# Performance work log

Hardware: AMD Instinct MI355X
Metric: run time of the kernel (lower is better)

The kernel has to match this reference:

```python
import jax, jax.numpy as jnp
import numpy as np

B, T, L = 64, 60, 49
EMBED, HID, VOCAB = 768, 768, 10000


def setup_inputs() -> dict:
    key = jax.random.key(0)
    ks = jax.random.split(key, 17)
    def n(k, shape, s=1.0):
        return jax.random.normal(k, shape, dtype=jnp.float32) * s
    W = 0.02  # param init scale
    return {
        "x": n(ks[0], (B, T, 2 * EMBED)),
        "hiddens": n(ks[1], (B, T, HID)),
        "cells": n(ks[2], (B, T, HID)),
        "G": n(ks[3], (B, L, HID)),
        "H": n(ks[4], (B, L, HID)),
        # Sentinel params (bias=False)
        "W_sx": n(ks[5], (HID, 2 * EMBED), W),
        "W_sh": n(ks[6], (HID, HID), W),
        # SwitchableAttention params
        "W_ax": n(ks[7], (HID, 2 * EMBED), W),
        "W_ah": n(ks[8], (HID, HID), W),
        "W_ag": n(ks[9], (HID, HID), W),
        "w_switch": n(ks[10], (1, HID), W),
        # Atten (adaptive attention) params, bias=False
        "Wv": n(ks[11], (L, HID), W),
        "Wg": n(ks[12], (L, HID), W),
        "Ws": n(ks[13], (L, HID), W),
        "wh": n(ks[14], (1, L), W),
        # output MLP
        "W_mlp": n(ks[15], (VOCAB, HID), W),
        "b_mlp": jnp.zeros((VOCAB,), dtype=jnp.float32),
    }


def reference(x, hiddens, cells, G, H, W_sx, W_sh, W_ax, W_ah, W_ag,
              w_switch, Wv, Wg, Ws, wh, W_mlp, b_mlp):
    # Dropout layers are treated as identity (eval mode).
    b, t, _ = x.shape
    # h_{t-1}: zero initial hidden prepended, last step dropped
    h0 = jnp.zeros((b, 1, HID), dtype=hiddens.dtype)
    hiddens_t_1 = jnp.concatenate([h0, hiddens[:, :-1, :]], axis=1)

    # Sentinel gate: sigmoid(Wx x + Wh h_{t-1}) * tanh(c_t)
    gate = jax.nn.sigmoid(jnp.einsum('bte,he->bth', x, W_sx)
                          + jnp.einsum('btk,hk->bth', hiddens_t_1, W_sh))
    s_t = gate * jnp.tanh(cells)  # [B,T,HID]

    # SwitchableAttention: gate between visual H and guidance G per region,
    # conditioned on pooled word context x.
    q = jnp.einsum('bte,he->bth', x, W_ax).mean(axis=1)  # [B,HID]
    sH = jnp.einsum('blh,oh->blo', jnp.tanh(jnp.einsum('blh,kh->blk', H, W_ah) + q[:, None, :]), w_switch)  # [B,L,1]
    sG = jnp.einsum('blh,oh->blo', jnp.tanh(jnp.einsum('blh,kh->blk', G, W_ag) + q[:, None, :]), w_switch)  # [B,L,1]
    switch_weights = jax.nn.softmax(jnp.concatenate([sH, sG], axis=-1), axis=-1)  # [B,L,2]
    V = switch_weights[..., 0:1] * H + switch_weights[..., 1:2] * G  # [B,L,HID]

    # Adaptive attention (Atten): spatial attention + visual sentinel
    pv = jnp.einsum('blh,kh->blk', V, Wv)        # [B,L,49]
    pg = jnp.einsum('bth,kh->btk', hiddens, Wg)  # [B,T,49]
    z_t = jnp.einsum('btlk,ok->btlo', jnp.tanh(pv[:, None, :, :] + pg[:, :, None, :]), wh)[..., 0]  # [B,T,L]
    alpha = jax.nn.softmax(z_t, axis=-1)  # [B,T,L]
    z_s = jnp.einsum('btk,ok->bto', jnp.tanh(jnp.einsum('bth,kh->btk', s_t, Ws) + pg), wh)  # [B,T,1]
    alpha_hat = jax.nn.softmax(jnp.concatenate([z_t, z_s], axis=-1), axis=-1)  # [B,T,L+1]
    beta = alpha_hat[..., -1:]  # [B,T,1]
    c_t = jnp.einsum('btl,blh->bth', alpha, V)
    c_hat = beta * s_t + (1.0 - beta) * c_t

    scores = jnp.einsum('bth,vh->btv', c_hat + hiddens, W_mlp) + b_mlp  # [B,T,VOCAB]
    return scores, alpha, beta, switch_weights
```

## Files before the change

### kernel.cpp

```cpp
#include <hip/hip_runtime.h>

#define BB 64
#define TT 60
#define LL 49
#define HID 768
#define E2 1536
#define VOC 10000
#define BT (BB*TT)
#define BL (BB*LL)
#define NPAD_MLP 10240
#define NPAD_S 128

typedef __bf16 bf16x8 __attribute__((ext_vector_type(8)));
typedef float f32x4 __attribute__((ext_vector_type(4)));

__device__ __forceinline__ unsigned short f2bf(float f) {
  union { float f; unsigned int u; } v; v.f = f;
  unsigned int u = v.u;
  return (unsigned short)((u + 0x7fffu + ((u >> 16) & 1u)) >> 16);
}
__device__ __forceinline__ float bf2f(unsigned short h) {
  union { unsigned int u; float f; } v; v.u = ((unsigned int)h) << 16;
  return v.f;
}
__device__ __forceinline__ float fast_tanh(float x) {
  float e = __expf(2.f * x);
  return 1.f - 2.f / (e + 1.f);
}
__device__ __forceinline__ float fast_sigmoid(float x) {
  return 1.f / (1.f + __expf(-x));
}

#define NSEG 14
#define CHUNK4 2048
struct SegT {
  const float* src;
  unsigned short* dst;
  int n4;
  int nrows;
  int mode;
  int blk0;
};
struct SegTable { SegT s[NSEG]; };

__global__ __launch_bounds__(256) void k_convall(SegTable tab) {
  int b = blockIdx.x;
  int si = 0;
#pragma unroll
  for (int i = 1; i < NSEG; ++i) si += (b >= tab.s[i].blk0);
  SegT sg = tab.s[si];
  int lb = b - sg.blk0;
  int end = (lb + 1) * CHUNK4; end = end < sg.n4 ? end : sg.n4;
  for (int i = lb * CHUNK4 + threadIdx.x; i < end; i += 256) {
    ushort4 o; o.x = o.y = o.z = o.w = 0;
    if (sg.mode == 0) {
      float4 v = ((const float4*)sg.src)[i];
      o.x = f2bf(v.x); o.y = f2bf(v.y); o.z = f2bf(v.z); o.w = f2bf(v.w);
    } else if (sg.mode == 1) {
      int row = i / 192;
      if (row < sg.nrows) {
        float4 v = ((const float4*)sg.src)[i];
        o.x = f2bf(v.x); o.y = f2bf(v.y); o.z = f2bf(v.z); o.w = f2bf(v.w);
      }
    } else {
      int bt = i / 192;
      if (bt % TT != 0) {
        float4 v = ((const float4*)sg.src)[i - 192];
        o.x = f2bf(v.x); o.y = f2bf(v.y); o.z = f2bf(v.z); o.w = f2bf(v.w);
      }
    }
    ((ushort4*)sg.dst)[i] = o;
  }
}

__global__ __launch_bounds__(256) void k_xmean(const float* __restrict__ x,
                                               unsigned short* __restrict__ xm) {
  int b = blockIdx.x / 6;
  int c = (blockIdx.x % 6) * 256 + threadIdx.x;
  float s = 0.f;
  for (int t = 0; t < TT; ++t) s += x[((size_t)b * TT + t) * E2 + c];
  xm[(size_t)b * E2 + c] = f2bf(s * (1.f / 60.f));
}

struct SSeg {
  const unsigned short* A; const unsigned short* B; float* C;
  int M, Nout, K, nMblk, blk0;
};
#define NSSEG 3
struct SSegTable { SSeg s[NSSEG]; };

__global__ __launch_bounds__(256) void gemm_bt_seg(SSegTable tab)
{
  __shared__ __attribute__((aligned(16))) unsigned short As[128*32];
  __shared__ __attribute__((aligned(16))) unsigned short Bs[128*32];
  const int tid  = threadIdx.x;
  const int lane = tid & 63;
  const int wave = tid >> 6;

  const int nwg = gridDim.x;
  const int id  = blockIdx.x;
  const int q = nwg >> 3, r = nwg & 7;
  const int xcd = id & 7, lo = id >> 3;
  const int wgid = (xcd < r ? xcd * (q + 1) : r * (q + 1) + (xcd - r) * q) + lo;

  int si = 0;
#pragma unroll
  for (int i = 1; i < NSSEG; ++i) si += (wgid >= tab.s[i].blk0);
  const SSeg sg = tab.s[si];
  const int lwg = wgid - sg.blk0;
  const int mb = lwg % sg.nMblk;
  const int nb = lwg / sg.nMblk;
  const int M = sg.M, Nout = sg.Nout, K = sg.K;
  const unsigned short* __restrict__ A  = sg.A;
  const unsigned short* __restrict__ Bw = sg.B;
  float* __restrict__ C = sg.C;
  const int m0 = mb * 128;
  const int n0 = nb * 128;
  const int wm = (wave >> 1) * 64;
  const int wn = (wave & 1) * 64;

  f32x4 acc[4][4];
#pragma unroll
  for (int i = 0; i < 4; ++i)
#pragma unroll
    for (int j = 0; j < 4; ++j) acc[i][j] = f32x4{0.f, 0.f, 0.f, 0.f};

  const int lrow = lane & 15;
  const int kb   = (lane >> 4) * 8;

  for (int k0 = 0; k0 < K; k0 += 32) {
    __syncthreads();
#pragma unroll
    for (int p = 0; p < 2; ++p) {
      int slot = p * 256 + wave * 64 + lane;
      int row = slot >> 2, c8 = slot & 3;
      int ar = m0 + row; ar = ar < M ? ar : (M - 1);
      const unsigned short* asrc = A + (size_t)ar * K + k0 + c8 * 8;
      __builtin_amdgcn_global_load_lds(
          (const __attribute__((address_space(1))) void*)asrc,
          (__attribute__((address_space(3))) void*)&As[(p * 256 + wave * 64) * 8],
          16, 0, 0);
      const unsigned short* bsrc = Bw + (size_t)(n0 + row) * K + k0 + c8 * 8;
      __builtin_amdgcn_global_load_lds(
          (const __attribute__((address_space(1))) void*)bsrc,
          (__attribute__((address_space(3))) void*)&Bs[(p * 256 + wave * 64) * 8],
          16, 0, 0);
    }
    __syncthreads();

    bf16x8 av[4], bv[4];
#pragma unroll
    for (int i = 0; i < 4; ++i)
      av[i] = *(const bf16x8*)&As[(wm + i * 16 + lrow) * 32 + kb];
#pragma unroll
    for (int j = 0; j < 4; ++j)
      bv[j] = *(const bf16x8*)&Bs[(wn + j * 16 + lrow) * 32 + kb];
#pragma unroll
    for (int i = 0; i < 4; ++i)
#pragma unroll
      for (int j = 0; j < 4; ++j)
        acc[i][j] = __builtin_amdgcn_mfma_f32_16x16x32_bf16(av[i], bv[j], acc[i][j], 0, 0, 0);
  }

  const int cr = (lane >> 4) * 4;
  const int cc = lane & 15;
#pragma unroll
  for (int i = 0; i < 4; ++i) {
    int row0 = m0 + wm + i * 16 + cr;
#pragma unroll
    for (int j = 0; j < 4; ++j) {
      int col = n0 + wn + j * 16 + cc;
      if (col < Nout) {
#pragma unroll
        for (int r2 = 0; r2 < 4; ++r2) {
          int row = row0 + r2;
          if (row < M) C[(size_t)row * Nout + col] = acc[i][j][r2];
        }
      }
    }
  }
}

#define BARR() do { asm volatile("" ::: "memory"); __builtin_amdgcn_s_barrier(); \
                    asm volatile("" ::: "memory"); } while (0)
#define VM4() asm volatile("s_waitcnt vmcnt(4)" ::: "memory")
#define VM0() asm volatile("s_waitcnt vmcnt(0)" ::: "memory")

#define STAGE1(bufi, op, kt) do {                                               \
  int k0_ = (kt) * 32;                                                          \
  _Pragma("unroll")                                                             \
  for (int l_ = 0; l_ < 2; ++l_) {                                              \
    int rr_ = l_ * 128 + sr0;                                                   \
    int ss_ = ssp ^ ((rr_ >> 1) & 3);                                           \
    int gr_;                                                                    \
    if (op) gr_ = n0 + rr_;                                                     \
    else    gr_ = CLAMP ? ((m0 + rr_) < M ? (m0 + rr_) : (M - 1)) : (m0 + rr_); \
    const unsigned short* src_ = ((op) ? Bw : Ap) + (size_t)gr_ * K + k0_ + ss_ * 8; \
    char* dst_ = smem + (bufi) * 32768 + (op) * 16384 + l_ * 8192 + w * 1024;   \
    __builtin_amdgcn_global_load_lds(                                           \
        (const __attribute__((address_space(1))) void*)src_,                    \
        (__attribute__((address_space(3))) void*)dst_, 16, 0, 0);               \
  }                                                                             \
} while (0)

#define LDA(bufi, row) (*(const bf16x8*)(smem + (bufi) * 32768 + (row) * 64 + (cg ^ (((row) >> 1) & 3)) * 16))
#define LDB(bufi, row) (*(const bf16x8*)(smem + (bufi) * 32768 + 16384 + (row) * 64 + (cg ^ (((row) >> 1) & 3)) * 16))

#define PH0(bufi, STAGE_STMT) do {                                              \
  STAGE_STMT;                                                                   \
  bfr0 = LDB(bufi, wn + lrow);                                                  \
  bfr1 = LDB(bufi, wn + 16 + lrow);                                             \
  _Pragma("unroll")                                                             \
  for (int i_ = 0; i_ < 8; ++i_) afr[i_] = LDA(bufi, wm + i_ * 16 + lrow);      \
  __builtin_amdgcn_s_setprio(1);                                                \
  _Pragma("unroll")                                                             \
  for (int i_ = 0; i_ < 8; ++i_) {                                              \
    acc[i_][0] = __builtin_amdgcn_mfma_f32_16x16x32_bf16(afr[i_], bfr0, acc[i_][0], 0, 0, 0); \
    acc[i_][1] = __builtin_amdgcn_mfma_f32_16x16x32_bf16(afr[i_], bfr1, acc[i_][1], 0, 0, 0); \
  }                                                                             \
  __builtin_amdgcn_s_setprio(0);                                                \
  BARR();                                                                       \
} while (0)

#define PH1(bufi, STAGE_STMT, VM_STMT) do {                                     \
  STAGE_STMT;                                                                   \
  bfr0 = LDB(bufi, wn + 32 + lrow);                                             \
  bfr1 = LDB(bufi, wn + 48 + lrow);                                             \
  __builtin_amdgcn_s_setprio(1);                                                \
  _Pragma("unroll")                                                             \
  for (int i_ = 0; i_ < 8; ++i_) {                                              \
    acc[i_][2] = __builtin_amdgcn_mfma_f32_16x16x32_bf16(afr[i_], bfr0, acc[i_][2], 0, 0, 0); \
    acc[i_][3] = __builtin_amdgcn_mfma_f32_16x16x32_bf16(afr[i_], bfr1, acc[i_][3], 0, 0, 0); \
  }                                                                             \
  __builtin_amdgcn_s_setprio(0);                                                \
  VM_STMT;                                                                      \
  BARR();                                                                       \
} while (0)

struct GSeg {
  const unsigned short* A; const unsigned short* B; float* C;
  const float* bias;
  int M, Nout, K, nMblk, blk0;
};
#define NGSEG 5
struct GSegTable { GSeg s[NGSEG]; };

template <bool CLAMP>
__global__ __launch_bounds__(512, 2) void gemm8p(GSegTable tab)
{
  extern __shared__ char smem[];
  const int tid  = threadIdx.x;
  const int lane = tid & 63;
  const int w    = tid >> 6;
  const int lrow = lane & 15;
  const int cg   = lane >> 4;
  const int sr0  = w * 16 + (lane >> 2);
  const int ssp  = lane & 3;

  const int nwg = gridDim.x;
  const int id  = blockIdx.x;
  const int q = nwg >> 3, r = nwg & 7;
  const int xcd = id & 7, lo = id >> 3;
  const int wgid = (xcd < r ? xcd * (q + 1) : r * (q + 1) + (xcd - r) * q) + lo;

  int si = 0;
#pragma unroll
  for (int i = 1; i < NGSEG; ++i) si += (wgid >= tab.s[i].blk0);
  const GSeg sg = tab.s[si];
  const int lwg = wgid - sg.blk0;
  const int mb = lwg % sg.nMblk;
  const int nb = lwg / sg.nMblk;
  const int M = sg.M, Nout = sg.Nout, K = sg.K;
  const unsigned short* __restrict__ Ap = sg.A;
  const unsigned short* __restrict__ Bw = sg.B;
  float* __restrict__ C = sg.C;
  const float* __restrict__ bias = sg.bias;

  const int m0 = mb * 256;
  const int n0 = nb * 256;
  const int wm = (w >> 2) * 128;
  const int wn = (w & 3) * 64;

  f32x4 acc[8][4];
#pragma unroll
  for (int i = 0; i < 8; ++i)
#pragma unroll
    for (int j = 0; j < 4; ++j) acc[i][j] = f32x4{0.f, 0.f, 0.f, 0.f};
  bf16x8 afr[8];
  bf16x8 bfr0, bfr1;

  const int NT = K >> 5;

  STAGE1(0, 0, 0);
  STAGE1(0, 1, 0);
  STAGE1(1, 0, 1);
  STAGE1(1, 1, 1);
  VM4();
  BARR();

  int b = 0;
  for (int kt = 0; kt < NT - 2; ++kt) {
    int b2 = b + 2; if (b2 >= 3) b2 -= 3;
    PH0(b, STAGE1(b2, 0, kt + 2));
    PH1(b, STAGE1(b2, 1, kt + 2), VM4(););
    ++b; if (b == 3) b = 0;
  }
  PH0(b, ;);
  PH1(b, ;, VM0(););
  ++b; if (b == 3) b = 0;
  PH0(b, ;);
  {
    bfr0 = LDB(b, wn + 32 + lrow);
    bfr1 = LDB(b, wn + 48 + lrow);
#pragma unroll
    for (int i_ = 0; i_ < 8; ++i_) {
      acc[i_][2] = __builtin_amdgcn_mfma_f32_16x16x32_bf16(afr[i_], bfr0, acc[i_][2], 0, 0, 0);
      acc[i_][3] = __builtin_amdgcn_mfma_f32_16x16x32_bf16(afr[i_], bfr1, acc[i_][3], 0, 0, 0);
    }
  }

#pragma unroll
  for (int i = 0; i < 8; ++i) {
    int row0 = m0 + wm + i * 16 + (lane >> 4) * 4;
#pragma unroll
    for (int j = 0; j < 4; ++j) {
      int col = n0 + wn + j * 16 + (lane & 15);
      if (col < Nout) {
        float badd = bias ? bias[col] : 0.f;
#pragma unroll
        for (int r2 = 0; r2 < 4; ++r2) {
          int row = row0 + r2;
          if (!CLAMP || row < M) C[(size_t)row * Nout + col] = acc[i][j][r2] + badd;
        }
      }
    }
  }
}

__global__ void k_st(const float* __restrict__ XS, const float* __restrict__ HS,
                     const float* __restrict__ cells, unsigned short* __restrict__ stbf, int n) {
  int i = blockIdx.x * blockDim.x + threadIdx.x;
  int stride = gridDim.x * blockDim.x;
  for (; i < n; i += stride) {
    float pre = XS[i] + HS[i];
    float v = fast_sigmoid(pre) * fast_tanh(cells[i]);
    stbf[i] = f2bf(v);
  }
}

__global__ __launch_bounds__(256) void k_switch(
    const float* __restrict__ AH, const float* __restrict__ AG,
    const float* __restrict__ q, const float* __restrict__ wsw,
    const float* __restrict__ H, const float* __restrict__ G,
    unsigned short* __restrict__ Vbf, float* __restrict__ sw_out)
{
  int bl = blockIdx.x;
  int b = bl / LL;
  int tid = threadIdx.x;
  float aH = 0.f, aG = 0.f;
  for (int h = tid; h < HID; h += 256) {
    float qv = q[b * HID + h], w = wsw[h];
    aH += fast_tanh(AH[(size_t)bl * HID + h] + qv) * w;
    aG += fast_tanh(AG[(size_t)bl * HID + h] + qv) * w;
  }
#pragma unroll
  for (int off = 32; off > 0; off >>= 1) {
    aH += __shfl_down(aH, off);
    aG += __shfl_down(aG, off);
  }
  __shared__ float redH[4], redG[4];
  int lane = tid & 63, wave = tid >> 6;
  if (lane == 0) { redH[wave] = aH; redG[wave] = aG; }
  __syncthreads();
  float sH = redH[0] + redH[1] + redH[2] + redH[3];
  float sG = redG[0] + redG[1] + redG[2] + redG[3];
  float m = fmaxf(sH, sG);
  float e0 = __expf(sH - m), e1 = __expf(sG - m);
  float inv = 1.f / (e0 + e1);
  float sw0 = e0 * inv, sw1 = e1 * inv;
  if (tid == 0) { sw_out[bl * 2] = sw0; sw_out[bl * 2 + 1] = sw1; }
  for (int h = tid; h < HID; h += 256) {
    float v = sw0 * H[(size_t)bl * HID + h] + sw1 * G[(size_t)bl * HID + h];
    Vbf[(size_t)bl * HID + h] = f2bf(v);
  }
}

__global__ __launch_bounds__(256) void k_attn(
    const float* __restrict__ PV, const float* __restrict__ PG,
    const float* __restrict__ SS, const float* __restrict__ wh,
    const unsigned short* __restrict__ stbf, const unsigned short* __restrict__ Vbf,
    const float* __restrict__ hiddens,
    float* __restrict__ alpha_out, float* __restrict__ beta_out,
    unsigned short* __restrict__ chh)
{
  const int TG = 4;
  int b  = blockIdx.x / (TT / TG);
  int t0 = (blockIdx.x % (TT / TG)) * TG;
  int tid = threadIdx.x;
  __shared__ float pg_s[TG][LL], wh_s[LL], zz[TG][LL + 1], alpha_s[TG][LL], beta_sh[TG];

  if (tid < LL) wh_s[tid] = wh[tid];
  if (tid < TG * LL) {
    int tt = tid / LL, k = tid - tt * LL;
    pg_s[tt][k] = PG[(size_t)(b * TT + t0 + tt) * 64 + k];
  }
  __syncthreads();

  if (tid < TG * (LL + 1)) {
    int tt = tid / (LL + 1), l = tid - tt * (LL + 1);
    const float* src = (l < LL) ? &PV[((size_t)b * LL + l) * 64]
                                : &SS[(size_t)(b * TT + t0 + tt) * 64];
    float acc = 0.f;
    for (int k = 0; k < LL; ++k) acc += fast_tanh(src[k] + pg_s[tt][k]) * wh_s[k];
    zz[tt][l] = acc;
  }
  __syncthreads();

  if (tid < TG) {
    int tt = tid, bt = b * TT + t0 + tt;
    float mx = -1e30f;
    for (int l = 0; l < LL; ++l) mx = fmaxf(mx, zz[tt][l]);
    float sum = 0.f;
    for (int l = 0; l < LL; ++l) { float e = __expf(zz[tt][l] - mx); alpha_s[tt][l] = e; sum += e; }
    float inv = 1.f / sum;
    for (int l = 0; l < LL; ++l) {
      alpha_s[tt][l] *= inv;
      alpha_out[(size_t)bt * LL + l] = alpha_s[tt][l];
    }
    float mx2 = fmaxf(mx, zz[tt][LL]);
    float s2 = 0.f;
    for (int l = 0; l <= LL; ++l) s2 += __expf(zz[tt][l] - mx2);
    float bet = __expf(zz[tt][LL] - mx2) / s2;
    beta_sh[tt] = bet;
    beta_out[bt] = bet;
  }
  __syncthreads();

  for (int h = tid; h < HID; h += 256) {
    float ct[TG] = {0.f, 0.f, 0.f, 0.f};
    for (int l = 0; l < LL; ++l) {
      float v = bf2f(Vbf[((size_t)b * LL + l) * HID + h]);
#pragma unroll
      for (int tt = 0; tt < TG; ++tt) ct[tt] += alpha_s[tt][l] * v;
    }
#pragma unroll
    for (int tt = 0; tt < TG; ++tt) {
      int bt = b * TT + t0 + tt;
      float bet = beta_sh[tt];
      float s = bf2f(stbf[(size_t)bt * HID + h]);
      float chat = bet * s + (1.f - bet) * ct[tt];
      chh[(size_t)bt * HID + h] = f2bf(chat + hiddens[(size_t)bt * HID + h]);
    }
  }
}

static inline int nblk(long n) {
  long g = (n + 255) / 256;
  if (g > 8192) g = 8192;
  return (int)g;
}

extern "C" void kernel_launch(void* const* d_in, const int* in_sizes, int n_in,
                              void* d_out, int out_size, void* d_ws, size_t ws_size,
                              hipStream_t stream)
{
  const float* x       = (const float*)d_in[0];
  const float* hiddens = (const float*)d_in[1];
  const float* cells   = (const float*)d_in[2];
  const float* G       = (const float*)d_in[3];
  const float* H       = (const float*)d_in[4];
  const float* W_sx    = (const float*)d_in[5];
  const float* W_sh    = (const float*)d_in[6];
  const float* W_ax    = (const float*)d_in[7];
  const float* W_ah    = (const float*)d_in[8];
  const float* W_ag    = (const float*)d_in[9];
  const float* w_sw    = (const float*)d_in[10];
  const float* Wv      = (const float*)d_in[11];
  const float* Wg      = (const float*)d_in[12];
  const float* Ws      = (const float*)d_in[13];
  const float* wh      = (const float*)d_in[14];
  const float* W_mlp   = (const float*)d_in[15];
  const float* b_mlp   = (const float*)d_in[16];

  float* scores = (float*)d_out;
  float* alpha  = scores + (size_t)BT * VOC;
  float* beta   = alpha + (size_t)BT * LL;
  float* swout  = beta + BT;

  char* wsp = (char*)d_ws;
  size_t off = 0;
  auto alloc = [&](size_t bytes) -> char* {
    char* p = wsp + off;
    off += (bytes + 255) & ~(size_t)255;
    return p;
  };

  unsigned short* xbf    = (unsigned short*)alloc((size_t)BT * E2 * 2);
  unsigned short* wsa    = (unsigned short*)alloc((size_t)E2 * E2 * 2);
  unsigned short* hprev  = (unsigned short*)alloc((size_t)BT * HID * 2);
  unsigned short* wshb   = (unsigned short*)alloc((size_t)HID * HID * 2);
  unsigned short* wahb   = (unsigned short*)alloc((size_t)HID * HID * 2);
  unsigned short* wagb   = (unsigned short*)alloc((size_t)HID * HID * 2);
  unsigned short* Hbf    = (unsigned short*)alloc((size_t)BL * HID * 2);
  unsigned short* Gbf    = (unsigned short*)alloc((size_t)BL * HID * 2);
  unsigned short* hidbf  = (unsigned short*)alloc((size_t)BT * HID * 2);
  unsigned short* wvb    = (unsigned short*)alloc((size_t)NPAD_S * HID * 2);
  unsigned short* wgb    = (unsigned short*)alloc((size_t)NPAD_S * HID * 2);
  unsigned short* wsb    = (unsigned short*)alloc((size_t)NPAD_S * HID * 2);
  unsigned short* wmlpb  = (unsigned short*)alloc((size_t)NPAD_MLP * HID * 2);
  unsigned short* Vbf    = (unsigned short*)alloc((size_t)BL * HID * 2);
  unsigned short* stbf   = (unsigned short*)alloc((size_t)BT * HID * 2);
  unsigned short* chh    = (unsigned short*)alloc((size_t)BT * HID * 2);
  unsigned short* xmbf   = (unsigned short*)alloc((size_t)BB * E2 * 2);
  float* XS = (float*)alloc((size_t)BT * HID * 4);
  float* HS = (float*)alloc((size_t)BT * HID * 4);
  float* AH = (float*)alloc((size_t)BL * HID * 4);
  float* AG = (float*)alloc((size_t)BL * HID * 4);
  float* qb = (float*)alloc((size_t)BB * HID * 4);
  float* PV = (float*)alloc((size_t)BL * 64 * 4);
  float* PG = (float*)alloc((size_t)BT * 64 * 4);
  float* SS = (float*)alloc((size_t)BT * 64 * 4);
  (void)ws_size; (void)in_sizes; (void)n_in; (void)out_size;

  SegTable tab;
  int blk = 0, si = 0;
  auto seg = [&](const float* s, unsigned short* d, int n4, int nrows, int mode) {
    tab.s[si].src = s; tab.s[si].dst = d; tab.s[si].n4 = n4;
    tab.s[si].nrows = nrows; tab.s[si].mode = mode; tab.s[si].blk0 = blk;
    blk += (n4 + CHUNK4 - 1) / CHUNK4; ++si;
  };
  seg(W_sx, wsa,                        HID * E2 / 4, 0, 0);
  seg(W_ax, wsa + (size_t)HID * E2,     HID * E2 / 4, 0, 0);
  seg(x, xbf,                           BT * E2 / 4, 0, 0);
  seg(hiddens, hprev,                   BT * HID / 4, 0, 2);
  seg(W_sh, wshb,                       HID * HID / 4, 0, 0);
  seg(W_ah, wahb,                       HID * HID / 4, 0, 0);
  seg(W_ag, wagb,                       HID * HID / 4, 0, 0);
  seg(H, Hbf,                           BL * HID / 4, 0, 0);
  seg(G, Gbf,                           BL * HID / 4, 0, 0);
  seg(hiddens, hidbf,                   BT * HID / 4, 0, 0);
  seg(Wv, wvb,                          NPAD_S * HID / 4, LL, 1);
  seg(Wg, wgb,                          NPAD_S * HID / 4, LL, 1);
  seg(Ws, wsb,                          NPAD_S * HID / 4, LL, 1);
  seg(W_mlp, wmlpb,                     NPAD_MLP * HID / 4, VOC, 1);
  k_convall<<<blk, 256, 0, stream>>>(tab);

  k_xmean<<<BB * 6, 256, 0, stream>>>(x, xmbf);

  GSegTable gt;
  int gblk = 0, gi = 0;
  auto gseg = [&](const unsigned short* A, const unsigned short* B, float* C,
                  const float* bias, int M, int N, int K, int nMblk, int nNblk) {
    gt.s[gi].A = A; gt.s[gi].B = B; gt.s[gi].C = C; gt.s[gi].bias = bias;
    gt.s[gi].M = M; gt.s[gi].Nout = N; gt.s[gi].K = K; gt.s[gi].nMblk = nMblk;
    gt.s[gi].blk0 = gblk;
    gblk += nMblk * nNblk; ++gi;
  };
  gseg(xbf,   wsa,                      XS, nullptr, BT, HID, E2,  15, 3);
  gseg(hprev, wshb,                     HS, nullptr, BT, HID, HID, 15, 3);
  gseg(Hbf,   wahb,                     AH, nullptr, BL, HID, HID, 13, 3);
  gseg(Gbf,   wagb,                     AG, nullptr, BL, HID, HID, 13, 3);
  gseg(xmbf,  wsa + (size_t)HID * E2,   qb, nullptr, BB, HID, E2,  1,  3);
  gemm8p<true><<<gblk, 512, 98304, stream>>>(gt);

  k_st<<<nblk((long)BT * HID), 256, 0, stream>>>(XS, HS, cells, stbf, BT * HID);
  k_switch<<<BL, 256, 0, stream>>>(AH, AG, qb, w_sw, H, G, Vbf, swout);

  SSegTable st;
  st.s[0] = SSeg{Vbf,   wvb, PV, BL, 64, HID, 25, 0};
  st.s[1] = SSeg{hidbf, wgb, PG, BT, 64, HID, 30, 25};
  st.s[2] = SSeg{stbf,  wsb, SS, BT, 64, HID, 30, 55};
  gemm_bt_seg<<<85, 256, 0, stream>>>(st);

  k_attn<<<BB * (TT / 4), 256, 0, stream>>>(PV, PG, SS, wh, stbf, Vbf, hiddens,
                                            alpha, beta, chh);

  GSegTable gs;
  for (int i = 0; i < NGSEG; ++i) { gs.s[i].blk0 = 0x7fffffff; gs.s[i].A = chh; gs.s[i].B = wmlpb; gs.s[i].C = scores; gs.s[i].bias = b_mlp; gs.s[i].M = BT; gs.s[i].Nout = VOC; gs.s[i].K = HID; gs.s[i].nMblk = 15; }
  gs.s[0].blk0 = 0;
  gemm8p<false><<<15 * 40, 512, 98304, stream>>>(gs);
}
```

Measured before the change: 292.6 us.

## Shrink GEMM tile to 256x128 and single-phase K loop

Changes the gemm8p tile from 256x256 to 256x128 output, so each warp computes 128x32 and keeps half as many accumulators. The B stage loads one row slice per thread, and the two-phase PH0/PH1 loop becomes a single TILE step that loads A fragments inline. LDS drops to 72KB and launch bounds ask for 4 blocks per CU, which doubles the grid for both the fused projection GEMM and the output MLP GEMM. The aim is higher occupancy and better wave balance across CUs, at the cost of lower arithmetic intensity and more A-tile reloads from global memory.

```diff
diff --git a/kernel.cpp b/kernel.cpp
--- a/kernel.cpp
+++ b/kernel.cpp
@@ -183,54 +183,48 @@
 
 #define BARR() do { asm volatile("" ::: "memory"); __builtin_amdgcn_s_barrier(); \
                     asm volatile("" ::: "memory"); } while (0)
-#define VM4() asm volatile("s_waitcnt vmcnt(4)" ::: "memory")
+#define VM3() asm volatile("s_waitcnt vmcnt(3)" ::: "memory")
 #define VM0() asm volatile("s_waitcnt vmcnt(0)" ::: "memory")
 
-#define STAGE1(bufi, op, kt) do {                                               \
+#define STAGE_A(bufi, kt) do {                                                  \
   int k0_ = (kt) * 32;                                                          \
   _Pragma("unroll")                                                             \
   for (int l_ = 0; l_ < 2; ++l_) {                                              \
     int rr_ = l_ * 128 + sr0;                                                   \
     int ss_ = ssp ^ ((rr_ >> 1) & 3);                                           \
-    int gr_;                                                                    \
-    if (op) gr_ = n0 + rr_;                                                     \
-    else    gr_ = CLAMP ? ((m0 + rr_) < M ? (m0 + rr_) : (M - 1)) : (m0 + rr_); \
-    const unsigned short* src_ = ((op) ? Bw : Ap) + (size_t)gr_ * K + k0_ + ss_ * 8; \
-    char* dst_ = smem + (bufi) * 32768 + (op) * 16384 + l_ * 8192 + w * 1024;   \
+    int gr_ = CLAMP ? ((m0 + rr_) < M ? (m0 + rr_) : (M - 1)) : (m0 + rr_);     \
+    const unsigned short* src_ = Ap + (size_t)gr_ * K + k0_ + ss_ * 8;          \
+    char* dst_ = smem + (bufi) * 24576 + l_ * 8192 + w * 1024;                  \
     __builtin_amdgcn_global_load_lds(                                           \
         (const __attribute__((address_space(1))) void*)src_,                    \
         (__attribute__((address_space(3))) void*)dst_, 16, 0, 0);               \
   }                                                                             \
 } while (0)
 
-#define LDA(bufi, row) (*(const bf16x8*)(smem + (bufi) * 32768 + (row) * 64 + (cg ^ (((row) >> 1) & 3)) * 16))
-#define LDB(bufi, row) (*(const bf16x8*)(smem + (bufi) * 32768 + 16384 + (row) * 64 + (cg ^ (((row) >> 1) & 3)) * 16))
-
-#define PH0(bufi, STAGE_STMT) do {                                              \
+#define STAGE_B(bufi, kt) do {                                                  \
+  int k0_ = (kt) * 32;                                                          \
+  int rr_ = sr0;                                                                \
+  int ss_ = ssp ^ ((rr_ >> 1) & 3);                                             \
+  const unsigned short* src_ = Bw + (size_t)(n0 + rr_) * K + k0_ + ss_ * 8;     \
+  char* dst_ = smem + (bufi) * 24576 + 16384 + w * 1024;                        \
+  __builtin_amdgcn_global_load_lds(                                             \
+      (const __attribute__((address_space(1))) void*)src_,                      \
+      (__attribute__((address_space(3))) void*)dst_, 16, 0, 0);                 \
+} while (0)
+
+#define LDA(bufi, row) (*(const bf16x8*)(smem + (bufi) * 24576 + (row) * 64 + (cg ^ (((row) >> 1) & 3)) * 16))
+#define LDB(bufi, row) (*(const bf16x8*)(smem + (bufi) * 24576 + 16384 + (row) * 64 + (cg ^ (((row) >> 1) & 3)) * 16))
+
+#define TILE(bufi, STAGE_STMT, VM_STMT) do {                                    \
   STAGE_STMT;                                                                   \
-  bfr0 = LDB(bufi, wn + lrow);                                                  \
-  bfr1 = LDB(bufi, wn + 16 + lrow);                                             \
-  _Pragma("unroll")                                                             \
-  for (int i_ = 0; i_ < 8; ++i_) afr[i_] = LDA(bufi, wm + i_ * 16 + lrow);      \
+  bf16x8 bfr0 = LDB(bufi, wn + lrow);                                           \
+  bf16x8 bfr1 = LDB(bufi, wn + 16 + lrow);                                      \
   __builtin_amdgcn_s_setprio(1);                                                \
   _Pragma("unroll")                                                             \
   for (int i_ = 0; i_ < 8; ++i_) {                                              \
-    acc[i_][0] = __builtin_amdgcn_mfma_f32_16x16x32_bf16(afr[i_], bfr0, acc[i_][0], 0, 0, 0); \
-    acc[i_][1] = __builtin_amdgcn_mfma_f32_16x16x32_bf16(afr[i_], bfr1, acc[i_][1], 0, 0, 0); \
-  }                                                                             \
-  __builtin_amdgcn_s_setprio(0);                                                \
-  BARR();                                                                       \
-} while (0)
-
-#define PH1(bufi, STAGE_STMT, VM_STMT) do {                                     \
-  STAGE_STMT;                                                                   \
-  bfr0 = LDB(bufi, wn + 32 + lrow);                                             \
-  bfr1 = LDB(bufi, wn + 48 + lrow);                                             \
-  __builtin_amdgcn_s_setprio(1);                                                \
-  _Pragma("unroll")                                                             \
-  for (int i_ = 0; i_ < 8; ++i_) {                                              \
-    acc[i_][2] = __builtin_amdgcn_mfma_f32_16x16x32_bf16(afr[i_], bfr0, acc[i_][2], 0, 0, 0); \
-    acc[i_][3] = __builtin_amdgcn_mfma_f32_16x16x32_bf16(afr[i_], bfr1, acc[i_][3], 0, 0, 0); \
+    bf16x8 a_ = LDA(bufi, wm + i_ * 16 + lrow);                                 \
+    acc[i_][0] = __builtin_amdgcn_mfma_f32_16x16x32_bf16(a_, bfr0, acc[i_][0], 0, 0, 0); \
+    acc[i_][1] = __builtin_amdgcn_mfma_f32_16x16x32_bf16(a_, bfr1, acc[i_][1], 0, 0, 0); \
   }                                                                             \
   __builtin_amdgcn_s_setprio(0);                                                \
   VM_STMT;                                                                      \
@@ -246,7 +240,7 @@
 struct GSegTable { GSeg s[NGSEG]; };
 
 template <bool CLAMP>
-__global__ __launch_bounds__(512, 2) void gemm8p(GSegTable tab)
+__global__ __launch_bounds__(512, 4) void gemm8p(GSegTable tab)
 {
   extern __shared__ char smem[];
   const int tid  = threadIdx.x;
@@ -277,53 +271,40 @@
   const float* __restrict__ bias = sg.bias;
 
   const int m0 = mb * 256;
-  const int n0 = nb * 256;
+  const int n0 = nb * 128;
   const int wm = (w >> 2) * 128;
-  const int wn = (w & 3) * 64;
-
-  f32x4 acc[8][4];
+  const int wn = (w & 3) * 32;
+
+  f32x4 acc[8][2];
 #pragma unroll
   for (int i = 0; i < 8; ++i)
 #pragma unroll
-    for (int j = 0; j < 4; ++j) acc[i][j] = f32x4{0.f, 0.f, 0.f, 0.f};
-  bf16x8 afr[8];
-  bf16x8 bfr0, bfr1;
+    for (int j = 0; j < 2; ++j) acc[i][j] = f32x4{0.f, 0.f, 0.f, 0.f};
 
   const int NT = K >> 5;
 
-  STAGE1(0, 0, 0);
-  STAGE1(0, 1, 0);
-  STAGE1(1, 0, 1);
-  STAGE1(1, 1, 1);
-  VM4();
+  STAGE_A(0, 0);
+  STAGE_B(0, 0);
+  STAGE_A(1, 1);
+  STAGE_B(1, 1);
+  VM3();
   BARR();
 
   int b = 0;
   for (int kt = 0; kt < NT - 2; ++kt) {
     int b2 = b + 2; if (b2 >= 3) b2 -= 3;
-    PH0(b, STAGE1(b2, 0, kt + 2));
-    PH1(b, STAGE1(b2, 1, kt + 2), VM4(););
+    TILE(b, { STAGE_A(b2, kt + 2); STAGE_B(b2, kt + 2); }, VM3(););
     ++b; if (b == 3) b = 0;
   }
-  PH0(b, ;);
-  PH1(b, ;, VM0(););
+  TILE(b, ;, VM0(););
   ++b; if (b == 3) b = 0;
-  PH0(b, ;);
-  {
-    bfr0 = LDB(b, wn + 32 + lrow);
-    bfr1 = LDB(b, wn + 48 + lrow);
-#pragma unroll
-    for (int i_ = 0; i_ < 8; ++i_) {
-      acc[i_][2] = __builtin_amdgcn_mfma_f32_16x16x32_bf16(afr[i_], bfr0, acc[i_][2], 0, 0, 0);
-      acc[i_][3] = __builtin_amdgcn_mfma_f32_16x16x32_bf16(afr[i_], bfr1, acc[i_][3], 0, 0, 0);
-    }
-  }
+  TILE(b, ;, ;);
 
 #pragma unroll
   for (int i = 0; i < 8; ++i) {
     int row0 = m0 + wm + i * 16 + (lane >> 4) * 4;
 #pragma unroll
-    for (int j = 0; j < 4; ++j) {
+    for (int j = 0; j < 2; ++j) {
       int col = n0 + wn + j * 16 + (lane & 15);
       if (col < Nout) {
         float badd = bias ? bias[col] : 0.f;
@@ -556,12 +537,12 @@
     gt.s[gi].blk0 = gblk;
     gblk += nMblk * nNblk; ++gi;
   };
-  gseg(xbf,   wsa,                      XS, nullptr, BT, HID, E2,  15, 3);
-  gseg(hprev, wshb,                     HS, nullptr, BT, HID, HID, 15, 3);
-  gseg(Hbf,   wahb,                     AH, nullptr, BL, HID, HID, 13, 3);
-  gseg(Gbf,   wagb,                     AG, nullptr, BL, HID, HID, 13, 3);
-  gseg(xmbf,  wsa + (size_t)HID * E2,   qb, nullptr, BB, HID, E2,  1,  3);
-  gemm8p<true><<<gblk, 512, 98304, stream>>>(gt);
+  gseg(xbf,   wsa,                      XS, nullptr, BT, HID, E2,  15, 6);
+  gseg(hprev, wshb,                     HS, nullptr, BT, HID, HID, 15, 6);
+  gseg(Hbf,   wahb,                     AH, nullptr, BL, HID, HID, 13, 6);
+  gseg(Gbf,   wagb,                     AG, nullptr, BL, HID, HID, 13, 6);
+  gseg(xmbf,  wsa + (size_t)HID * E2,   qb, nullptr, BB, HID, E2,  1,  6);
+  gemm8p<true><<<gblk, 512, 73728, stream>>>(gt);
 
   k_st<<<nblk((long)BT * HID), 256, 0, stream>>>(XS, HS, cells, stbf, BT * HID);
   k_switch<<<BL, 256, 0, stream>>>(AH, AG, qb, w_sw, H, G, Vbf, swout);
@@ -578,5 +559,5 @@
   GSegTable gs;
   for (int i = 0; i < NGSEG; ++i) { gs.s[i].blk0 = 0x7fffffff; gs.s[i].A = chh; gs.s[i].B = wmlpb; gs.s[i].C = scores; gs.s[i].bias = b_mlp; gs.s[i].M = BT; gs.s[i].Nout = VOC; gs.s[i].K = HID; gs.s[i].nMblk = 15; }
   gs.s[0].blk0 = 0;
-  gemm8p<false><<<15 * 40, 512, 98304, stream>>>(gs);
-}
+  gemm8p<false><<<15 * 80, 512, 73728, stream>>>(gs);
+}
```

Result: no change. 293.6 us (+0.3%).
